# Optimization experiments

Hardware: AMD Instinct MI355X
Metric: run time of the kernel (lower is better)

The kernel has to match this reference:

```python
import jax, jax.numpy as jnp
import numpy as np

N = 100_000   # nodes
E = 3_200_000 # edges
F = 13        # input features
H = 64        # hidden dim
G = 512       # graphs in batch
C = 2         # output classes
BN_EPS = 1e-5


def _linear(key, fan_in, fan_out):
    kw, kb = jax.random.split(key)
    bound = 1.0 / np.sqrt(fan_in)
    W = jax.random.uniform(kw, (fan_in, fan_out), jnp.float32, -bound, bound)
    b = jax.random.uniform(kb, (fan_out,), jnp.float32, -bound, bound)
    return W, b


def _conv_params(key, fin, fout):
    k1, k2, k3 = jax.random.split(key, 3)
    W1, b1 = _linear(k1, fin, fout)
    W2, b2 = _linear(k2, fout, fout)
    gamma = jnp.ones((fout,), jnp.float32)
    beta = jnp.zeros((fout,), jnp.float32)
    mean = jax.random.normal(k3, (fout,), jnp.float32) * 0.1
    var = jnp.ones((fout,), jnp.float32)
    return W1, b1, gamma, beta, mean, var, W2, b2


def setup_inputs() -> dict:
    key = jax.random.key(0)
    ks = jax.random.split(key, 10)
    x = jax.random.normal(ks[0], (N, F), jnp.float32)
    src = jax.random.randint(ks[1], (E,), 0, N, jnp.int32)
    dst = jax.random.randint(ks[2], (E,), 0, N, jnp.int32)
    batch = jnp.sort(jax.random.randint(ks[3], (N,), 0, G, jnp.int32))
    inp = {"x": x, "src": src, "dst": dst, "batch": batch}
    for i, name in enumerate(["c1", "c2", "c3"]):
        fin = F if i == 0 else H
        W1, b1, g, be, m, v, W2, b2 = _conv_params(ks[4 + i], fin, H)
        inp.update({f"{name}_W1": W1, f"{name}_b1": b1, f"{name}_g": g,
                    f"{name}_be": be, f"{name}_m": m, f"{name}_v": v,
                    f"{name}_W2": W2, f"{name}_b2": b2})
    inp["fc1_W"], inp["fc1_b"] = _linear(ks[7], 3 * H, 3 * H)
    inp["fc2_W"], inp["fc2_b"] = _linear(ks[8], 3 * H, C)
    return inp


def _mlp(h, W1, b1, g, be, m, v, W2, b2):
    # Linear -> BatchNorm1d (inference, running stats) -> ReLU -> Linear -> ReLU
    h = h @ W1 + b1
    h = (h - m) * jax.lax.rsqrt(v + BN_EPS) * g + be
    h = jax.nn.relu(h)
    return jax.nn.relu(h @ W2 + b2)


def _gin_conv(x, src, dst, mlp_params):
    # GINConv with eps=0: MLP(x + sum_{j->i} x_j) via scatter-add over edges
    agg = jax.ops.segment_sum(x[src], dst, num_segments=N)
    return _mlp(x + agg, *mlp_params)


def reference(x, src, dst, batch,
              c1_W1, c1_b1, c1_g, c1_be, c1_m, c1_v, c1_W2, c1_b2,
              c2_W1, c2_b1, c2_g, c2_be, c2_m, c2_v, c2_W2, c2_b2,
              c3_W1, c3_b1, c3_g, c3_be, c3_m, c3_v, c3_W2, c3_b2,
              fc1_W, fc1_b, fc2_W, fc2_b):
    h1 = jax.nn.relu(_gin_conv(x, src, dst, (c1_W1, c1_b1, c1_g, c1_be, c1_m, c1_v, c1_W2, c1_b2)))
    h2 = jax.nn.relu(_gin_conv(h1, src, dst, (c2_W1, c2_b1, c2_g, c2_be, c2_m, c2_v, c2_W2, c2_b2)))
    h3 = jax.nn.relu(_gin_conv(h2, src, dst, (c3_W1, c3_b1, c3_g, c3_be, c3_m, c3_v, c3_W2, c3_b2)))
    p1 = jax.ops.segment_sum(h1, batch, num_segments=G)
    p2 = jax.ops.segment_sum(h2, batch, num_segments=G)
    p3 = jax.ops.segment_sum(h3, batch, num_segments=G)
    h = jnp.concatenate([p1, p2, p3], axis=1)  # [G, 3H]
    h = jax.nn.relu(h @ fc1_W + fc1_b)
    # Dropout is identity in eval mode
    h = h @ fc2_W + fc2_b
    return jax.nn.log_softmax(h, axis=-1)
```

## Files before the change

kernel.cpp:

```cpp
#include <hip/hip_runtime.h>

#define NNODES 100000
#define NEDGES 3200000
#define NF 13
#define NFP 16
#define NG 512
#define BN_EPS 1e-5f
#define NTILES (NNODES / 16)
#define CAP 72

#define BSH 9
#define NBUCK ((NNODES + 511) / 512)
#define RCAP 18500
#define PTILE 4096
#define NPBLK ((NEDGES + PTILE - 1) / PTILE)

typedef __attribute__((ext_vector_type(8))) short bf16x8;
typedef __attribute__((ext_vector_type(4))) float f32x4;

__device__ __forceinline__ float bf2f(unsigned short u) {
    return __uint_as_float(((unsigned)u) << 16);
}
__device__ __forceinline__ unsigned short f2bf(float f) {
    unsigned u = __float_as_uint(f);
    unsigned r = (u + 0x7FFFu + ((u >> 16) & 1u)) >> 16;
    return (unsigned short)r;
}

__launch_bounds__(256)
__global__ void partition_kernel(const int* __restrict__ src, const int* __restrict__ dst,
                                 int* __restrict__ gcount, int* __restrict__ pairbuf) {
    __shared__ int lhist[NBUCK];
    __shared__ int lbase[NBUCK];
    __shared__ int lpos[NBUCK];
    int t = threadIdx.x;
    int base = blockIdx.x * PTILE;
    int cnt = NEDGES - base; if (cnt > PTILE) cnt = PTILE;

    int v[PTILE / 256], b[PTILE / 256];
#pragma unroll
    for (int j = 0; j < PTILE / 256; ++j) {
        int i = t + j * 256;
        if (i < cnt) {
            int d = __builtin_nontemporal_load(dst + base + i);
            int s = __builtin_nontemporal_load(src + base + i);
            b[j] = d >> BSH;
            v[j] = ((d & 511) << 17) | s;
        } else b[j] = -1;
    }
    if (t < NBUCK) lhist[t] = 0;
    __syncthreads();
#pragma unroll
    for (int j = 0; j < PTILE / 256; ++j)
        if (b[j] >= 0) atomicAdd(&lhist[b[j]], 1);
    __syncthreads();
    if (t < NBUCK) {
        lbase[t] = atomicAdd(&gcount[t], lhist[t]);
        lpos[t] = 0;
    }
    __syncthreads();
#pragma unroll
    for (int j = 0; j < PTILE / 256; ++j) {
        if (b[j] >= 0) {
            int p = atomicAdd(&lpos[b[j]], 1);
            pairbuf[(size_t)b[j] * RCAP + lbase[b[j]] + p] = v[j];
        }
    }
}

__launch_bounds__(512)
__global__ void bucket_scatter_kernel(const int* __restrict__ pairbuf,
                                      const int* __restrict__ gcount,
                                      int* __restrict__ cursor, int* __restrict__ csr) {
    __shared__ int lcnt[512];
    int bk = blockIdx.x;
    int lo = bk << BSH;
    int cnt = gcount[bk];
    if (threadIdx.x < 512) lcnt[threadIdx.x] = 0;
    __syncthreads();
    const int* pb = pairbuf + (size_t)bk * RCAP;
    for (int i = threadIdx.x; i < cnt; i += 512) {
        int p = pb[i];
        int s = p & 0x1FFFF;
        int dl = p >> 17;
        int pos = atomicAdd(&lcnt[dl], 1);
        csr[(size_t)(lo + dl) * CAP + pos] = s;
    }
    __syncthreads();
    int n = lo + threadIdx.x;
    if (threadIdx.x < 512 && n < NNODES) cursor[n] = n * CAP + lcnt[threadIdx.x];
}

__global__ void cvt_x_kernel(const float* __restrict__ x, unsigned short* __restrict__ xbf) {
    const int total = NNODES * NFP;
    int idx = blockIdx.x * blockDim.x + threadIdx.x;
    int stride = gridDim.x * blockDim.x;
    for (int i = idx; i < total; i += stride) {
        int n = i >> 4;
        int f = i & 15;
        xbf[i] = (f < NF) ? f2bf(x[n * NF + f]) : (unsigned short)0;
    }
}

__global__ void build_frags_kernel(const float* __restrict__ w10, const float* __restrict__ w20,
                                   const float* __restrict__ w11, const float* __restrict__ w21,
                                   const float* __restrict__ w12, const float* __restrict__ w22,
                                   unsigned short* __restrict__ wfrag) {
    int tid = blockIdx.x * blockDim.x + threadIdx.x;
    if (tid >= 3072) return;
    int layer = tid >> 10;
    int rem = tid & 1023;
    int mat = rem >> 9;
    int tile = (rem >> 7) & 3;
    int chunk = (rem >> 6) & 1;
    int lane = rem & 63;
    int quad = lane >> 4, n = lane & 15;
    const float* W = (layer == 0) ? (mat ? w20 : w10)
                   : (layer == 1) ? (mat ? w21 : w11)
                                  : (mat ? w22 : w12);
    int K = (layer == 0 && mat == 0) ? NF : 64;
    unsigned short* o = wfrag + ((size_t)tid) * 8;
#pragma unroll
    for (int j = 0; j < 8; ++j) {
        int k = chunk * 32 + quad * 8 + j;
        float val = (k < K) ? W[k * 64 + tile * 16 + n] : 0.f;
        o[j] = f2bf(val);
    }
}

template <int FSTR, int RL, int UNROLL, int PADZ>
__launch_bounds__(256, 8)
__global__ void agg_vec_kernel(const unsigned short* __restrict__ xin,
                               const int* __restrict__ cursor,
                               const int* __restrict__ csr,
                               unsigned short* __restrict__ y) {
    const int EPG = 64 / RL;
    int lane = threadIdx.x & 63;
    int g = lane / RL;
    int r = lane % RL;
    int wave = (blockIdx.x * blockDim.x + threadIdx.x) >> 6;
    int nw = (gridDim.x * blockDim.x) >> 6;

    for (int n = wave; n < NNODES; n += nw) {
        int beg = n * CAP;
        int end = cursor[n];
        float ax = 0.f, ay = 0.f, az = 0.f, aw = 0.f;
        if (g == 0) {
            ushort4 u = *(const ushort4*)&xin[n * FSTR + r * 4];
            ax = bf2f(u.x); ay = bf2f(u.y); az = bf2f(u.z); aw = bf2f(u.w);
        }
        int j = beg;
        const int STEP = UNROLL * EPG;
        for (; j + STEP <= end; j += STEP) {
#pragma unroll
            for (int t = 0; t < UNROLL; ++t) {
                int e = j + t * EPG + g;
                int i0 = csr[e];
                ushort4 u = *(const ushort4*)&xin[i0 * FSTR + r * 4];
                ax += bf2f(u.x); ay += bf2f(u.y); az += bf2f(u.z); aw += bf2f(u.w);
            }
        }
        for (; j < end; j += EPG) {
            int e = j + g;
            if (e < end) {
                int i0 = csr[e];
                ushort4 u = *(const ushort4*)&xin[i0 * FSTR + r * 4];
                ax += bf2f(u.x); ay += bf2f(u.y); az += bf2f(u.z); aw += bf2f(u.w);
            }
        }
#pragma unroll
        for (int m = RL; m < 64; m <<= 1) {
            ax += __shfl_xor(ax, m, 64);
            ay += __shfl_xor(ay, m, 64);
            az += __shfl_xor(az, m, 64);
            aw += __shfl_xor(aw, m, 64);
        }
        if (g == 0) {
            ushort4 o;
            o.x = f2bf(ax); o.y = f2bf(ay); o.z = f2bf(az); o.w = f2bf(aw);
            *(ushort4*)&y[n * 64 + r * 4] = o;
        } else if (PADZ && g == 1) {
            ushort4 o; o.x = 0; o.y = 0; o.z = 0; o.w = 0;
            *(ushort4*)&y[n * 64 + 16 + r * 4] = o;
        }
    }
}

template <int KC1>
__launch_bounds__(256)
__global__ void mlp_mfma_kernel(const unsigned short* __restrict__ ybf,
                                const unsigned short* __restrict__ wfrag,
                                const float* __restrict__ b1, const float* __restrict__ g,
                                const float* __restrict__ be, const float* __restrict__ m,
                                const float* __restrict__ v,  const float* __restrict__ b2,
                                unsigned short* __restrict__ hout) {
    __shared__ __align__(16) unsigned short zs[4][16 * 72];
    int lane = threadIdx.x & 63;
    int wid = threadIdx.x >> 6;
    int quad = lane >> 4;
    int n16 = lane & 15;

    const bf16x8* wf = (const bf16x8*)wfrag;
    bf16x8 w1f[4][2], w2f[4][2];
#pragma unroll
    for (int t = 0; t < 4; ++t) {
#pragma unroll
        for (int c = 0; c < 2; ++c) {
            w1f[t][c] = wf[((0 * 4 + t) * 2 + c) * 64 + lane];
            w2f[t][c] = wf[((1 * 4 + t) * 2 + c) * 64 + lane];
        }
    }
    float scaleF[4], shiftF[4], b2F[4];
#pragma unroll
    for (int t = 0; t < 4; ++t) {
        int f = t * 16 + n16;
        float sc = g[f] * rsqrtf(v[f] + BN_EPS);
        scaleF[t] = sc;
        shiftF[t] = (b1[f] - m[f]) * sc + be[f];
        b2F[t] = b2[f];
    }

    unsigned short* zrow = &zs[wid][0];
    int ntiles = gridDim.x * 4;
    for (int tile = blockIdx.x * 4 + wid; tile < NTILES; tile += ntiles) {
        int nodebase = tile * 16;
        const unsigned short* yrow = ybf + (size_t)(nodebase + n16) * 64 + quad * 8;
        bf16x8 a0 = *(const bf16x8*)yrow;
        bf16x8 a1 = (KC1 == 2) ? *(const bf16x8*)(yrow + 32) : a0;

        f32x4 acc[4];
#pragma unroll
        for (int t = 0; t < 4; ++t) {
            f32x4 z4 = {0.f, 0.f, 0.f, 0.f};
            z4 = __builtin_amdgcn_mfma_f32_16x16x32_bf16(a0, w1f[t][0], z4, 0, 0, 0);
            if (KC1 == 2)
                z4 = __builtin_amdgcn_mfma_f32_16x16x32_bf16(a1, w1f[t][1], z4, 0, 0, 0);
            acc[t] = z4;
        }
#pragma unroll
        for (int t = 0; t < 4; ++t) {
#pragma unroll
            for (int r = 0; r < 4; ++r) {
                float z = fmaxf(fmaf(acc[t][r], scaleF[t], shiftF[t]), 0.f);
                zrow[(quad * 4 + r) * 72 + t * 16 + n16] = f2bf(z);
            }
        }
        __threadfence_block();
        bf16x8 az0 = *(const bf16x8*)&zrow[n16 * 72 + quad * 8];
        bf16x8 az1 = *(const bf16x8*)&zrow[n16 * 72 + 32 + quad * 8];

        f32x4 acc2[4];
#pragma unroll
        for (int t = 0; t < 4; ++t) {
            f32x4 z4 = {0.f, 0.f, 0.f, 0.f};
            z4 = __builtin_amdgcn_mfma_f32_16x16x32_bf16(az0, w2f[t][0], z4, 0, 0, 0);
            z4 = __builtin_amdgcn_mfma_f32_16x16x32_bf16(az1, w2f[t][1], z4, 0, 0, 0);
            acc2[t] = z4;
        }
#pragma unroll
        for (int t = 0; t < 4; ++t) {
#pragma unroll
            for (int r = 0; r < 4; ++r) {
                float h = fmaxf(acc2[t][r] + b2F[t], 0.f);
                hout[(size_t)(nodebase + quad * 4 + r) * 64 + t * 16 + n16] = f2bf(h);
            }
        }
        __threadfence_block();
    }
}

__global__ void pool_head_kernel(const unsigned short* __restrict__ h1,
                                 const unsigned short* __restrict__ h2,
                                 const unsigned short* __restrict__ h3,
                                 const int* __restrict__ batch,
                                 const float* __restrict__ fc1W, const float* __restrict__ fc1b,
                                 const float* __restrict__ fc2W, const float* __restrict__ fc2b,
                                 float* __restrict__ out) {
    __shared__ float ps[192];
    __shared__ float hs[192];
    __shared__ int bounds[2];
    int gi = blockIdx.x;
    int t = threadIdx.x;
    if (t < 2) {
        int target = gi + t;
        int lo = 0, hi = NNODES;
        while (lo < hi) {
            int mid = (lo + hi) >> 1;
            if (batch[mid] < target) lo = mid + 1; else hi = mid;
        }
        bounds[t] = lo;
    }
    __syncthreads();
    int nlo = bounds[0], nhi = bounds[1];
    const unsigned short* hb = (t < 64) ? h1 : (t < 128) ? h2 : h3;
    int f = t & 63;
    float s = 0.f;
    for (int n = nlo; n < nhi; ++n) s += bf2f(hb[n * 64 + f]);
    ps[t] = s;
    __syncthreads();
    float acc = fc1b[t];
#pragma unroll 8
    for (int k = 0; k < 192; ++k) acc = fmaf(ps[k], fc1W[k * 192 + t], acc);
    hs[t] = fmaxf(acc, 0.f);
    __syncthreads();
    if (t == 0) {
        float l0 = fc2b[0], l1 = fc2b[1];
        for (int k = 0; k < 192; ++k) {
            float h = hs[k];
            l0 = fmaf(h, fc2W[k * 2 + 0], l0);
            l1 = fmaf(h, fc2W[k * 2 + 1], l1);
        }
        float mx = fmaxf(l0, l1);
        float lse = mx + logf(expf(l0 - mx) + expf(l1 - mx));
        out[gi * 2 + 0] = l0 - lse;
        out[gi * 2 + 1] = l1 - lse;
    }
}

extern "C" void kernel_launch(void* const* d_in, const int* in_sizes, int n_in,
                              void* d_out, int out_size, void* d_ws, size_t ws_size,
                              hipStream_t stream) {
    const float* x = (const float*)d_in[0];
    const int* src = (const int*)d_in[1];
    const int* dst = (const int*)d_in[2];
    const int* batch = (const int*)d_in[3];
    const float* c1[8];
    const float* c2[8];
    const float* c3[8];
    for (int i = 0; i < 8; ++i) {
        c1[i] = (const float*)d_in[4 + i];
        c2[i] = (const float*)d_in[12 + i];
        c3[i] = (const float*)d_in[20 + i];
    }
    const float* fc1W = (const float*)d_in[28];
    const float* fc1b = (const float*)d_in[29];
    const float* fc2W = (const float*)d_in[30];
    const float* fc2b = (const float*)d_in[31];
    float* out = (float*)d_out;

    unsigned short* base = (unsigned short*)d_ws;
    const size_t NA = (size_t)NNODES * 64;
    unsigned short* ybf = base;
    unsigned short* xbf = ybf + NA;
    unsigned short* h1  = xbf + (size_t)NNODES * NFP;
    unsigned short* h2  = h1 + NA;
    unsigned short* h3  = h2 + NA;
    unsigned short* wfrag = h3 + NA;
    int* ibase = (int*)(wfrag + 3 * 8192);
    int* cursor  = ibase;
    int* gcount  = ibase + NNODES;
    int* csr     = gcount + NBUCK;
    int* pairbuf = csr + (size_t)NNODES * CAP + 256;

    hipMemsetAsync(gcount, 0, NBUCK * sizeof(int), stream);

    cvt_x_kernel<<<2048, 256, 0, stream>>>(x, xbf);
    build_frags_kernel<<<12, 256, 0, stream>>>(c1[0], c1[6], c2[0], c2[6], c3[0], c3[6], wfrag);
    partition_kernel<<<NPBLK, 256, 0, stream>>>(src, dst, gcount, pairbuf);
    bucket_scatter_kernel<<<NBUCK, 512, 0, stream>>>(pairbuf, gcount, cursor, csr);

    const int AGG_BLOCKS = 25000;
    const int MLP_BLOCKS = 1024;

    agg_vec_kernel<NFP, 4, 2, 1><<<AGG_BLOCKS, 256, 0, stream>>>(xbf, cursor, csr, ybf);
    mlp_mfma_kernel<1><<<MLP_BLOCKS, 256, 0, stream>>>(
        ybf, wfrag + 0 * 8192, c1[1], c1[2], c1[3], c1[4], c1[5], c1[7], h1);

    agg_vec_kernel<64, 16, 4, 0><<<AGG_BLOCKS, 256, 0, stream>>>(h1, cursor, csr, ybf);
    mlp_mfma_kernel<2><<<MLP_BLOCKS, 256, 0, stream>>>(
        ybf, wfrag + 1 * 8192, c2[1], c2[2], c2[3], c2[4], c2[5], c2[7], h2);

    agg_vec_kernel<64, 16, 4, 0><<<AGG_BLOCKS, 256, 0, stream>>>(h2, cursor, csr, ybf);
    mlp_mfma_kernel<2><<<MLP_BLOCKS, 256, 0, stream>>>(
        ybf, wfrag + 2 * 8192, c3[1], c3[2], c3[3], c3[4], c3[5], c3[7], h3);

    pool_head_kernel<<<NG, 192, 0, stream>>>(h1, h2, h3, batch, fc1W, fc1b, fc2W, fc2b, out);
}
```

Measured before the change: 452.3 us.

## Split pooling into chunked atomic segment-sum kernel and separate MLP head

```diff
diff --git a/kernel.cpp b/kernel.cpp
--- a/kernel.cpp
+++ b/kernel.cpp
@@ -14,6 +14,9 @@
 #define RCAP 18500
 #define PTILE 4096
 #define NPBLK ((NEDGES + PTILE - 1) / PTILE)
+
+#define NCHUNK ((NNODES + 63) / 64)
+#define NPTASK (3 * NCHUNK)
 
 typedef __attribute__((ext_vector_type(8))) short bf16x8;
 typedef __attribute__((ext_vector_type(4))) float f32x4;
@@ -269,34 +272,43 @@
     }
 }
 
-__global__ void pool_head_kernel(const unsigned short* __restrict__ h1,
-                                 const unsigned short* __restrict__ h2,
-                                 const unsigned short* __restrict__ h3,
-                                 const int* __restrict__ batch,
-                                 const float* __restrict__ fc1W, const float* __restrict__ fc1b,
-                                 const float* __restrict__ fc2W, const float* __restrict__ fc2b,
-                                 float* __restrict__ out) {
+__launch_bounds__(256)
+__global__ void pool_kernel(const unsigned short* __restrict__ h1,
+                            const unsigned short* __restrict__ h2,
+                            const unsigned short* __restrict__ h3,
+                            const int* __restrict__ batch,
+                            float* __restrict__ pool) {
+    int task = blockIdx.x * 4 + (threadIdx.x >> 6);
+    if (task >= NPTASK) return;
+    int lane = threadIdx.x & 63;
+    int layer = task / NCHUNK;
+    int c = task - layer * NCHUNK;
+    int n0 = c * 64;
+    int n1 = n0 + 64; if (n1 > NNODES) n1 = NNODES;
+    const unsigned short* hb = (layer == 0) ? h1 : (layer == 1) ? h2 : h3;
+    float acc = 0.f;
+    int curg = batch[n0];
+    for (int n = n0; n < n1; ++n) {
+        int gid = batch[n];
+        if (gid != curg) {
+            atomicAdd(&pool[(size_t)curg * 192 + layer * 64 + lane], acc);
+            acc = 0.f;
+            curg = gid;
+        }
+        acc += bf2f(hb[(size_t)n * 64 + lane]);
+    }
+    atomicAdd(&pool[(size_t)curg * 192 + layer * 64 + lane], acc);
+}
+
+__global__ void head_kernel(const float* __restrict__ pool,
+                            const float* __restrict__ fc1W, const float* __restrict__ fc1b,
+                            const float* __restrict__ fc2W, const float* __restrict__ fc2b,
+                            float* __restrict__ out) {
     __shared__ float ps[192];
     __shared__ float hs[192];
-    __shared__ int bounds[2];
     int gi = blockIdx.x;
     int t = threadIdx.x;
-    if (t < 2) {
-        int target = gi + t;
-        int lo = 0, hi = NNODES;
-        while (lo < hi) {
-            int mid = (lo + hi) >> 1;
-            if (batch[mid] < target) lo = mid + 1; else hi = mid;
-        }
-        bounds[t] = lo;
-    }
-    __syncthreads();
-    int nlo = bounds[0], nhi = bounds[1];
-    const unsigned short* hb = (t < 64) ? h1 : (t < 128) ? h2 : h3;
-    int f = t & 63;
-    float s = 0.f;
-    for (int n = nlo; n < nhi; ++n) s += bf2f(hb[n * 64 + f]);
-    ps[t] = s;
+    ps[t] = pool[gi * 192 + t];
     __syncthreads();
     float acc = fc1b[t];
 #pragma unroll 8
@@ -346,13 +358,15 @@
     unsigned short* h2  = h1 + NA;
     unsigned short* h3  = h2 + NA;
     unsigned short* wfrag = h3 + NA;
-    int* ibase = (int*)(wfrag + 3 * 8192);
+    float* pool = (float*)(wfrag + 3 * 8192);
+    int* ibase = (int*)(pool + (size_t)NG * 192);
     int* cursor  = ibase;
     int* gcount  = ibase + NNODES;
     int* csr     = gcount + NBUCK;
     int* pairbuf = csr + (size_t)NNODES * CAP + 256;
 
     hipMemsetAsync(gcount, 0, NBUCK * sizeof(int), stream);
+    hipMemsetAsync(pool, 0, (size_t)NG * 192 * sizeof(float), stream);
 
     cvt_x_kernel<<<2048, 256, 0, stream>>>(x, xbf);
     build_frags_kernel<<<12, 256, 0, stream>>>(c1[0], c1[6], c2[0], c2[6], c3[0], c3[6], wfrag);
@@ -374,5 +388,6 @@
     mlp_mfma_kernel<2><<<MLP_BLOCKS, 256, 0, stream>>>(
         ybf, wfrag + 2 * 8192, c3[1], c3[2], c3[3], c3[4], c3[5], c3[7], h3);
 
-    pool_head_kernel<<<NG, 192, 0, stream>>>(h1, h2, h3, batch, fc1W, fc1b, fc2W, fc2b, out);
-}
+    pool_kernel<<<(NPTASK + 3) / 4, 256, 0, stream>>>(h1, h2, h3, batch, pool);
+    head_kernel<<<NG, 192, 0, stream>>>(pool, fc1W, fc1b, fc2W, fc2b, out);
+}
```

Result: faster. 423.6 us (-6.3%).
